# Kernel optimization log

Measured on AMD Instinct MI355X. Metric: run time of the kernel, lower is better.

Reference implementation:

```python
import jax, jax.numpy as jnp
import numpy as np

B, ENC, NCLUST = 8192, 256, 32


def setup_inputs() -> dict:
    key = jax.random.key(0)
    k1, k2 = jax.random.split(key)
    encodings = jax.random.normal(k1, (B, ENC), dtype=jnp.float32)
    logits = jax.random.normal(k2, (B, NCLUST), dtype=jnp.float32) * 2.0
    categorical = jax.nn.softmax(logits, axis=1)
    return {"encodings": encodings, "categorical": categorical, "k": 25}


def reference(encodings, categorical, k):
    """Vectorized ClusterOverlap training-path math.

    Original layer is an identity on encodings; the regularizer/metric is the
    per-sample neighbourhood entropy weighted by cluster confidence. We return
    that [B] vector (the compute of interest; reduce_mean of it is the loss).
    """
    hard_groups = jnp.argmax(categorical, axis=1)          # [B] int
    max_groups = jnp.max(categorical, axis=1)              # [B]

    # Pairwise Euclidean distances via the GEMM identity (fused cdist).
    sq = jnp.sum(encodings * encodings, axis=1)            # [B]
    d2 = sq[:, None] + sq[None, :] - 2.0 * (encodings @ encodings.T)
    dist = jnp.sqrt(jnp.maximum(d2, 0.0))                  # [B, B]

    # max_distance = sort(distances)[k]; neighbourhood = distances < max_distance
    thr = jnp.sort(dist, axis=1)[:, k]                     # [B]
    mask = (dist < thr[:, None]).astype(jnp.float32)       # [B, B]
    n_neigh = jnp.sum(mask, axis=1)                        # [B] (~k, incl. self)

    # bincount of neighbour cluster ids per row: mask @ one_hot(hard_groups)
    onehot = jax.nn.one_hot(hard_groups, categorical.shape[1], dtype=jnp.float32)
    counts = mask @ onehot                                 # [B, C]
    bins = counts / n_neigh[:, None]
    entropy = -jnp.sum(bins * jnp.log(bins + 1e-5), axis=1)  # [B]

    return entropy * max_groups
```

## Files before the change

kernel.cpp:

```cpp
#include <hip/hip_runtime.h>
#include <math.h>

#define BN 8192
#define ENC 256
#define NCL 32
#define BM 256
#define BK 32
#define CCAP 1024
#define SCOL 2048
#define SN 256
#define RCAP 24

typedef __attribute__((ext_vector_type(8))) short short8;
typedef __attribute__((ext_vector_type(4))) float f32x4;
typedef __attribute__((ext_vector_type(4))) unsigned uint4v;

__device__ __forceinline__ ushort f2bf(float x) {
    unsigned b = __float_as_uint(x);
    return (ushort)((b + 0x7FFFu + ((b >> 16) & 1u)) >> 16);
}

__device__ __forceinline__ void async16(void* lds, const void* g) {
    __builtin_amdgcn_global_load_lds(
        (const __attribute__((address_space(1))) unsigned*)g,
        (__attribute__((address_space(3))) unsigned*)lds, 16, 0, 0);
}

__global__ void prep_kernel(const float* __restrict__ enc, const float* __restrict__ cat,
                            float* __restrict__ sq, float* __restrict__ maxg,
                            int* __restrict__ hard, ushort* __restrict__ eh,
                            ushort* __restrict__ el, int* __restrict__ ccnt) {
    int w = threadIdx.x >> 6, l = threadIdx.x & 63;
    int row = blockIdx.x * 4 + w;
    int gid = blockIdx.x * 256 + threadIdx.x;
    if (gid < BN) ccnt[gid] = 0;

    const float4* e4 = (const float4*)(enc + (size_t)row * ENC);
    float4 v = e4[l];
    float s = v.x * v.x + v.y * v.y + v.z * v.z + v.w * v.w;
    for (int m = 32; m; m >>= 1) s += __shfl_xor(s, m, 64);

    ushort4 hh, ll;
    hh.x = f2bf(v.x); ll.x = f2bf(v.x - __uint_as_float((unsigned)hh.x << 16));
    hh.y = f2bf(v.y); ll.y = f2bf(v.y - __uint_as_float((unsigned)hh.y << 16));
    hh.z = f2bf(v.z); ll.z = f2bf(v.z - __uint_as_float((unsigned)hh.z << 16));
    hh.w = f2bf(v.w); ll.w = f2bf(v.w - __uint_as_float((unsigned)hh.w << 16));
    int g = l >> 1;
    int gs = (g & ~3) | ((g & 3) ^ ((row >> 1) & 3));
    int kp = gs * 8 + (l & 1) * 4;
    *(ushort4*)(eh + (size_t)row * ENC + kp) = hh;
    *(ushort4*)(el + (size_t)row * ENC + kp) = ll;

    float cv = (l < NCL) ? cat[(size_t)row * NCL + l] : -__builtin_huge_valf();
    int ci = (l < NCL) ? l : 0x7fffffff;
    for (int m = 32; m; m >>= 1) {
        float ov = __shfl_xor(cv, m, 64);
        int oi = __shfl_xor(ci, m, 64);
        if (ov > cv || (ov == cv && oi < ci)) { cv = ov; ci = oi; }
    }
    if (l == 0) { sq[row] = s; maxg[row] = cv; hard[row] = ci; }
}

__global__ __launch_bounds__(512, 2)
void dist_mfma_kernel(const ushort* __restrict__ eh, const ushort* __restrict__ el,
                      const float* __restrict__ sq, int mode,
                      float* __restrict__ samp, const unsigned* __restrict__ piv,
                      unsigned* __restrict__ cval, int* __restrict__ cidxb,
                      int* __restrict__ ccnt) {
    __shared__ __align__(16) ushort lds0[2][4 * BM * BK];

    int t = threadIdx.x, l = t & 63;
    int w = t >> 6;
    int wm = w >> 2, wn = w & 3;

    int bx, by;
    if (mode) {
        int gx = gridDim.x;
        int bid = blockIdx.y * gx + blockIdx.x;
        int xcd = bid & 7, i = bid >> 3;
        int strip = gx >> 3;
        bx = xcd * strip + (i % strip);
        by = i / strip;
    } else { bx = blockIdx.x; by = blockIdx.y; }

    int gi0 = by * BM;
    int j0 = (mode ? 0 : SCOL) + bx * BM;

    f32x4 acc[8][4];
#pragma unroll
    for (int m = 0; m < 8; ++m)
#pragma unroll
        for (int n = 0; n < 4; ++n) acc[m][n] = (f32x4){0.f, 0.f, 0.f, 0.f};

    int srow = t >> 2;
    int sg = (t & 3) * 8;
    int il = l & 15;

#define STAGE(BUF, K0)                                                        \
    do {                                                                      \
        _Pragma("unroll") for (int q_ = 0; q_ < 2; ++q_) {                    \
            int r_ = srow + q_ * 128;                                         \
            size_t ga_ = (size_t)(gi0 + r_) * ENC + (K0) + sg;                \
            size_t gb_ = (size_t)(j0 + r_) * ENC + (K0) + sg;                 \
            int ldo_ = r_ * BK + sg;                                          \
            async16(&lds0[BUF][0 * BM * BK + ldo_], eh + ga_);                \
            async16(&lds0[BUF][1 * BM * BK + ldo_], el + ga_);                \
            async16(&lds0[BUF][2 * BM * BK + ldo_], eh + gb_);                \
            async16(&lds0[BUF][3 * BM * BK + ldo_], el + gb_);                \
        }                                                                     \
    } while (0)

    STAGE(0, 0);
    __syncthreads();

#pragma unroll
    for (int ks = 0; ks < 8; ++ks) {
        int cb = ks & 1;
        if (ks + 1 < 8) STAGE(cb ^ 1, (ks + 1) * BK);

        const ushort* Ah = &lds0[cb][0];
        const ushort* Al = Ah + BM * BK;
        const ushort* Bh = Ah + 2 * BM * BK;
        const ushort* Bl = Ah + 3 * BM * BK;

        short8 bh[4], bl4[4];
#pragma unroll
        for (int n = 0; n < 4; ++n) {
            int R = wn * 64 + n * 16 + il;
            int gl = (l >> 4) ^ ((R >> 1) & 3);
            bh[n]  = *(const short8*)(Bh + R * BK + gl * 8);
            bl4[n] = *(const short8*)(Bl + R * BK + gl * 8);
        }
#pragma unroll
        for (int m = 0; m < 8; ++m) {
            int Ra = wm * 128 + m * 16 + il;
            int gla = (l >> 4) ^ ((Ra >> 1) & 3);
            short8 am  = *(const short8*)(Ah + Ra * BK + gla * 8);
            short8 alm = *(const short8*)(Al + Ra * BK + gla * 8);
#pragma unroll
            for (int n = 0; n < 4; ++n) {
                acc[m][n] = __builtin_amdgcn_mfma_f32_16x16x32_bf16(bh[n],  am,  acc[m][n], 0, 0, 0);
                acc[m][n] = __builtin_amdgcn_mfma_f32_16x16x32_bf16(bl4[n], am,  acc[m][n], 0, 0, 0);
                acc[m][n] = __builtin_amdgcn_mfma_f32_16x16x32_bf16(bh[n],  alm, acc[m][n], 0, 0, 0);
            }
        }

        __syncthreads();
    }
#undef STAGE

    int q4 = (l >> 4) * 4;
    float sqi[8];
    float sqj[4][4];
#pragma unroll
    for (int m = 0; m < 8; ++m) sqi[m] = sq[gi0 + wm * 128 + m * 16 + il];
#pragma unroll
    for (int n = 0; n < 4; ++n)
#pragma unroll
        for (int r = 0; r < 4; ++r) sqj[n][r] = sq[j0 + wn * 64 + n * 16 + q4 + r];

    if (!mode) {
#pragma unroll
        for (int m = 0; m < 8; ++m)
#pragma unroll
            for (int n = 0; n < 4; ++n) {
                float4 o;
                o.x = fmaxf(sqi[m] + sqj[n][0] - 2.f * acc[m][n][0], 0.f);
                o.y = fmaxf(sqi[m] + sqj[n][1] - 2.f * acc[m][n][1], 0.f);
                o.z = fmaxf(sqi[m] + sqj[n][2] - 2.f * acc[m][n][2], 0.f);
                o.w = fmaxf(sqi[m] + sqj[n][3] - 2.f * acc[m][n][3], 0.f);
                int row = gi0 + wm * 128 + m * 16 + il;
                int jc = j0 + wn * 64 + n * 16 + q4;
                *(float4*)(samp + (size_t)row * SN + (jc - SCOL)) = o;
            }
        return;
    }

    int* rcnt = (int*)&lds0[0][0];
    int* rbase = rcnt + BM;
    unsigned* bval = (unsigned*)(rbase + BM);
    int* bidx = (int*)(bval + BM * RCAP);

    if (t < BM) rcnt[t] = 0;
    unsigned pv[8];
#pragma unroll
    for (int m = 0; m < 8; ++m) pv[m] = piv[gi0 + wm * 128 + m * 16 + il];
    __syncthreads();

#pragma unroll
    for (int m = 0; m < 8; ++m)
#pragma unroll
        for (int n = 0; n < 4; ++n) {
            int lr = wm * 128 + m * 16 + il;
            int jc = j0 + wn * 64 + n * 16 + q4;
#pragma unroll
            for (int r = 0; r < 4; ++r) {
                float o = fmaxf(sqi[m] + sqj[n][r] - 2.f * acc[m][n][r], 0.f);
                unsigned ub = __float_as_uint(o);
                if (ub < pv[m]) {
                    int pos = atomicAdd(&rcnt[lr], 1);
                    if (pos < RCAP) {
                        bval[lr * RCAP + pos] = ub;
                        bidx[lr * RCAP + pos] = jc + r;
                    } else {
                        int slot = atomicAdd(&ccnt[gi0 + lr], 1);
                        if (slot < CCAP) {
                            cval[(size_t)(gi0 + lr) * CCAP + slot] = ub;
                            cidxb[(size_t)(gi0 + lr) * CCAP + slot] = jc + r;
                        }
                    }
                }
            }
        }
    __syncthreads();

    if (t < BM) {
        int c = rcnt[t]; if (c > RCAP) c = RCAP;
        rbase[t] = c ? atomicAdd(&ccnt[gi0 + t], c) : 0;
    }
    __syncthreads();

    {
        int lr = t >> 1;
        int c = rcnt[lr]; if (c > RCAP) c = RCAP;
        int b = rbase[lr];
        for (int e = t & 1; e < c; e += 2) {
            int s = b + e;
            if (s < CCAP) {
                cval[(size_t)(gi0 + lr) * CCAP + s] = bval[lr * RCAP + e];
                cidxb[(size_t)(gi0 + lr) * CCAP + s] = bidx[lr * RCAP + e];
            }
        }
    }
}

__global__ void pivot_kernel(const float* __restrict__ samp, const int* __restrict__ kptr,
                             unsigned* __restrict__ piv) {
    int w = threadIdx.x >> 6, l = threadIdx.x & 63;
    int row = blockIdx.x * 4 + w;
    const uint4v* rd = (const uint4v*)(samp + (size_t)row * SN);
    uint4v sv = rd[l];

    int topn = *kptr + 1;
    int r = topn / 16 + 1; if (r < 8) r = 8;

    unsigned lo = 0u, hi = 0x7F800000u;
    while (lo < hi) {
        unsigned mid = lo + ((hi - lo) >> 1);
        int c = 0;
#pragma unroll
        for (int e = 0; e < 4; ++e) c += __popcll(__ballot(sv[e] <= mid));
        if (c >= r) hi = mid; else lo = mid + 1;
    }
    if (l == 0) piv[row] = lo;
}

__global__ __launch_bounds__(256, 2)
void select_kernel(const unsigned* __restrict__ cval, const int* __restrict__ cidxb,
                   const int* __restrict__ ccnt, const unsigned* __restrict__ piv,
                   const float* __restrict__ enc, const float* __restrict__ sq,
                   const float* __restrict__ maxg, const int* __restrict__ hard,
                   const int* __restrict__ kptr, float* __restrict__ out) {
    __shared__ __align__(16) unsigned sval[CCAP];
    __shared__ int sidx[CCAP];
    __shared__ __align__(16) unsigned rowbuf[BN];
    __shared__ __align__(16) float encrow[ENC];
    __shared__ int scnt[2][4];
    __shared__ int sbins[NCL];

    int t = threadIdx.x, w = t >> 6, l = t & 63;
    int li = blockIdx.x;
    if (t < NCL) sbins[t] = 0;

    int topn = *kptr + 1;
    int nc = ccnt[li];
    bool ok = (nc >= topn) && (nc <= CCAP);
    unsigned thr;

    if (ok) {
#pragma unroll
        for (int k2 = 0; k2 < 4; ++k2) sval[t + k2 * 256] = 0xFFFFFFFFu;
        for (int pos = t; pos < nc; pos += 256) {
            sval[pos] = cval[(size_t)li * CCAP + pos];
            sidx[pos] = cidxb[(size_t)li * CCAP + pos];
        }
        __syncthreads();

        int pp = 0;
        unsigned lo = 0u, hi = piv[li];
        while (lo < hi) {
            unsigned mid = lo + ((hi - lo) >> 1);
            uint4v cv = ((const uint4v*)sval)[t];
            int cnt = 0;
#pragma unroll
            for (int c = 0; c < 4; ++c) cnt += __popcll(__ballot(cv[c] <= mid));
            if (l == 0) scnt[pp][w] = cnt;
            __syncthreads();
            int tot = scnt[pp][0] + scnt[pp][1] + scnt[pp][2] + scnt[pp][3];
            if (tot >= topn) hi = mid; else lo = mid + 1;
            pp ^= 1;
        }
        thr = lo;

        for (int pos = t; pos < nc; pos += 256)
            if (sval[pos] < thr) atomicAdd(&sbins[hard[sidx[pos]]], 1);
    } else {
        if (t < 64) ((float4*)encrow)[t] = ((const float4*)(enc + (size_t)li * ENC))[t];
        __syncthreads();
        float sqi = sq[li];
        for (int c0 = 0; c0 < BN; c0 += 256) {
            int c = c0 + t;
            const float* ec = enc + (size_t)c * ENC;
            float dot = 0.f;
            for (int d = 0; d < ENC; ++d) dot = fmaf(encrow[d], ec[d], dot);
            rowbuf[c] = __float_as_uint(fmaxf(sqi + sq[c] - 2.f * dot, 0.f));
        }
        __syncthreads();

        int pp = 0;
        unsigned lo = 0u, hi = 0x7F800000u;
        while (lo < hi) {
            unsigned mid = lo + ((hi - lo) >> 1);
            int cnt = 0;
#pragma unroll
            for (int q = 0; q < 8; ++q) {
                uint4v u = ((const uint4v*)rowbuf)[q * 256 + t];
#pragma unroll
                for (int c = 0; c < 4; ++c) cnt += __popcll(__ballot(u[c] <= mid));
            }
            if (l == 0) scnt[pp][w] = cnt;
            __syncthreads();
            int tot = scnt[pp][0] + scnt[pp][1] + scnt[pp][2] + scnt[pp][3];
            if (tot >= topn) hi = mid; else lo = mid + 1;
            pp ^= 1;
        }
        thr = lo;

#pragma unroll
        for (int q = 0; q < 8; ++q) {
            uint4v u = ((const uint4v*)rowbuf)[q * 256 + t];
#pragma unroll
            for (int c = 0; c < 4; ++c)
                if (u[c] < thr)
                    atomicAdd(&sbins[hard[(q * 256 + t) * 4 + c]], 1);
        }
    }
    __syncthreads();

    if (t < NCL) {
        int cnt = sbins[t];
        int n = cnt;
        for (int m = 16; m; m >>= 1) n += __shfl_xor(n, m, 64);
        float nf = (float)n;
        float b = (float)cnt / nf;
        float term = -b * logf(b + 1e-5f);
        for (int m = 16; m; m >>= 1) term += __shfl_xor(term, m, 64);
        if (t == 0) out[li] = term * maxg[li];
    }
}

extern "C" void kernel_launch(void* const* d_in, const int* in_sizes, int n_in,
                              void* d_out, int out_size, void* d_ws, size_t ws_size,
                              hipStream_t stream) {
    const float* enc = (const float*)d_in[0];
    const float* cat = (const float*)d_in[1];
    const int* kptr = (const int*)d_in[2];
    float* out = (float*)d_out;

    float* sq = (float*)d_ws;
    float* maxg = sq + BN;
    int* hard = (int*)(maxg + BN);
    ushort* eh = (ushort*)(hard + BN);
    ushort* el = eh + (size_t)BN * ENC;
    float* samp = (float*)(el + (size_t)BN * ENC);
    unsigned* piv = (unsigned*)(samp + (size_t)BN * SN);
    int* ccnt = (int*)(piv + BN);
    unsigned* cval = (unsigned*)(ccnt + BN);
    int* cidxb = (int*)(cval + (size_t)BN * CCAP);

    prep_kernel<<<BN / 4, 256, 0, stream>>>(enc, cat, sq, maxg, hard, eh, el, ccnt);

    dim3 gs(SN / BM, BN / BM);
    dist_mfma_kernel<<<gs, 512, 0, stream>>>(eh, el, sq, 0, samp, piv, cval, cidxb, ccnt);

    pivot_kernel<<<BN / 4, 256, 0, stream>>>(samp, kptr, piv);

    dim3 gm(BN / BM, BN / BM);
    dist_mfma_kernel<<<gm, 512, 0, stream>>>(eh, el, sq, 1, samp, piv, cval, cidxb, ccnt);

    select_kernel<<<BN, 256, 0, stream>>>(cval, cidxb, ccnt, piv, enc, sq,
                                          maxg, hard, kptr, out);
}
```

Measured before the change: 315.4 us.

## Interleave GEMM LDS reads with async staging; one wave per row in select

The main distance GEMM loop is split into four phases. Each phase reads a pair of A fragments from LDS, issues half of the next tile's async global-to-LDS loads, and then runs an MFMA cluster at raised wave priority, with explicit barriers and waitcnts placed between phases. This spreads load issue across the compute instead of issuing it all up front. The select kernel now handles four rows per block, one wave per row, keeping candidates in registers and counting with wave-local ballots in place of block-wide barriers. Rows whose candidate count is out of range fall back to a serial per-block full-row path, which adds risk if there are many such rows.

```diff
diff --git a/kernel.cpp b/kernel.cpp
--- a/kernel.cpp
+++ b/kernel.cpp
@@ -96,28 +96,64 @@
     int sg = (t & 3) * 8;
     int il = l & 15;
 
-#define STAGE(BUF, K0)                                                        \
+#define STAGE_A(BUF, K0)                                                      \
     do {                                                                      \
         _Pragma("unroll") for (int q_ = 0; q_ < 2; ++q_) {                    \
             int r_ = srow + q_ * 128;                                         \
             size_t ga_ = (size_t)(gi0 + r_) * ENC + (K0) + sg;                \
-            size_t gb_ = (size_t)(j0 + r_) * ENC + (K0) + sg;                 \
             int ldo_ = r_ * BK + sg;                                          \
             async16(&lds0[BUF][0 * BM * BK + ldo_], eh + ga_);                \
             async16(&lds0[BUF][1 * BM * BK + ldo_], el + ga_);                \
+        }                                                                     \
+    } while (0)
+#define STAGE_B(BUF, K0)                                                      \
+    do {                                                                      \
+        _Pragma("unroll") for (int q_ = 0; q_ < 2; ++q_) {                    \
+            int r_ = srow + q_ * 128;                                         \
+            size_t gb_ = (size_t)(j0 + r_) * ENC + (K0) + sg;                 \
+            int ldo_ = r_ * BK + sg;                                          \
             async16(&lds0[BUF][2 * BM * BK + ldo_], eh + gb_);                \
             async16(&lds0[BUF][3 * BM * BK + ldo_], el + gb_);                \
         }                                                                     \
     } while (0)
 
-    STAGE(0, 0);
+#define READ_APAIR(PH, AHp, ALp)                                              \
+    short8 a##PH##h0, a##PH##h1, a##PH##l0, a##PH##l1;                        \
+    do {                                                                      \
+        int Ra0 = wm * 128 + (2 * PH) * 16 + il;                              \
+        int Ra1 = Ra0 + 16;                                                   \
+        int g0 = (l >> 4) ^ ((Ra0 >> 1) & 3);                                 \
+        int g1 = (l >> 4) ^ ((Ra1 >> 1) & 3);                                 \
+        a##PH##h0 = *(const short8*)(AHp + Ra0 * BK + g0 * 8);                \
+        a##PH##h1 = *(const short8*)(AHp + Ra1 * BK + g1 * 8);                \
+        a##PH##l0 = *(const short8*)(ALp + Ra0 * BK + g0 * 8);                \
+        a##PH##l1 = *(const short8*)(ALp + Ra1 * BK + g1 * 8);                \
+    } while (0)
+
+#define CLUSTER(PH)                                                           \
+    do {                                                                      \
+        _Pragma("unroll") for (int n_ = 0; n_ < 4; ++n_) {                    \
+            acc[2*PH][n_]   = __builtin_amdgcn_mfma_f32_16x16x32_bf16(bh[n_],  a##PH##h0, acc[2*PH][n_],   0, 0, 0); \
+            acc[2*PH][n_]   = __builtin_amdgcn_mfma_f32_16x16x32_bf16(bl4[n_], a##PH##h0, acc[2*PH][n_],   0, 0, 0); \
+            acc[2*PH][n_]   = __builtin_amdgcn_mfma_f32_16x16x32_bf16(bh[n_],  a##PH##l0, acc[2*PH][n_],   0, 0, 0); \
+            acc[2*PH+1][n_] = __builtin_amdgcn_mfma_f32_16x16x32_bf16(bh[n_],  a##PH##h1, acc[2*PH+1][n_], 0, 0, 0); \
+            acc[2*PH+1][n_] = __builtin_amdgcn_mfma_f32_16x16x32_bf16(bl4[n_], a##PH##h1, acc[2*PH+1][n_], 0, 0, 0); \
+            acc[2*PH+1][n_] = __builtin_amdgcn_mfma_f32_16x16x32_bf16(bh[n_],  a##PH##l1, acc[2*PH+1][n_], 0, 0, 0); \
+        }                                                                     \
+    } while (0)
+
+#define BAR()     __builtin_amdgcn_s_barrier()
+#define LGKM0()   do { asm volatile("s_waitcnt lgkmcnt(0)" ::: "memory");     \
+                       __builtin_amdgcn_sched_barrier(0); } while (0)
+#define VM0()     asm volatile("s_waitcnt vmcnt(0)" ::: "memory")
+
+    STAGE_A(0, 0);
+    STAGE_B(0, 0);
     __syncthreads();
 
 #pragma unroll
     for (int ks = 0; ks < 8; ++ks) {
-        int cb = ks & 1;
-        if (ks + 1 < 8) STAGE(cb ^ 1, (ks + 1) * BK);
-
+        const int cb = ks & 1, nb = cb ^ 1;
         const ushort* Ah = &lds0[cb][0];
         const ushort* Al = Ah + BM * BK;
         const ushort* Bh = Ah + 2 * BM * BK;
@@ -131,23 +167,30 @@
             bh[n]  = *(const short8*)(Bh + R * BK + gl * 8);
             bl4[n] = *(const short8*)(Bl + R * BK + gl * 8);
         }
-#pragma unroll
-        for (int m = 0; m < 8; ++m) {
-            int Ra = wm * 128 + m * 16 + il;
-            int gla = (l >> 4) ^ ((Ra >> 1) & 3);
-            short8 am  = *(const short8*)(Ah + Ra * BK + gla * 8);
-            short8 alm = *(const short8*)(Al + Ra * BK + gla * 8);
-#pragma unroll
-            for (int n = 0; n < 4; ++n) {
-                acc[m][n] = __builtin_amdgcn_mfma_f32_16x16x32_bf16(bh[n],  am,  acc[m][n], 0, 0, 0);
-                acc[m][n] = __builtin_amdgcn_mfma_f32_16x16x32_bf16(bl4[n], am,  acc[m][n], 0, 0, 0);
-                acc[m][n] = __builtin_amdgcn_mfma_f32_16x16x32_bf16(bh[n],  alm, acc[m][n], 0, 0, 0);
-            }
-        }
-
-        __syncthreads();
-    }
-#undef STAGE
+        READ_APAIR(0, Ah, Al);
+        if (ks + 1 < 8) STAGE_A(nb, (ks + 1) * BK);
+        BAR(); LGKM0();
+        __builtin_amdgcn_s_setprio(1); CLUSTER(0); __builtin_amdgcn_s_setprio(0);
+        BAR();
+        READ_APAIR(1, Ah, Al);
+        if (ks + 1 < 8) STAGE_B(nb, (ks + 1) * BK);
+        BAR(); LGKM0();
+        __builtin_amdgcn_s_setprio(1); CLUSTER(1); __builtin_amdgcn_s_setprio(0);
+        BAR();
+        READ_APAIR(2, Ah, Al);
+        BAR(); LGKM0();
+        __builtin_amdgcn_s_setprio(1); CLUSTER(2); __builtin_amdgcn_s_setprio(0);
+        BAR();
+        READ_APAIR(3, Ah, Al);
+        BAR(); LGKM0();
+        __builtin_amdgcn_s_setprio(1); CLUSTER(3); __builtin_amdgcn_s_setprio(0);
+        if (ks + 1 < 8) VM0();
+        BAR();
+    }
+#undef STAGE_A
+#undef STAGE_B
+#undef READ_APAIR
+#undef CLUSTER
 
     int q4 = (l >> 4) * 4;
     float sqi[8];
@@ -261,53 +304,53 @@
                    const float* __restrict__ enc, const float* __restrict__ sq,
                    const float* __restrict__ maxg, const int* __restrict__ hard,
                    const int* __restrict__ kptr, float* __restrict__ out) {
-    __shared__ __align__(16) unsigned sval[CCAP];
-    __shared__ int sidx[CCAP];
     __shared__ __align__(16) unsigned rowbuf[BN];
     __shared__ __align__(16) float encrow[ENC];
     __shared__ int scnt[2][4];
-    __shared__ int sbins[NCL];
+    __shared__ int sbins[4][NCL];
+    __shared__ int sfail;
 
     int t = threadIdx.x, w = t >> 6, l = t & 63;
-    int li = blockIdx.x;
-    if (t < NCL) sbins[t] = 0;
+    int li = blockIdx.x * 4 + w;
+    if (t == 0) sfail = 0;
+    if (l < NCL) sbins[w][l] = 0;
+    __syncthreads();
 
     int topn = *kptr + 1;
     int nc = ccnt[li];
     bool ok = (nc >= topn) && (nc <= CCAP);
-    unsigned thr;
 
     if (ok) {
-#pragma unroll
-        for (int k2 = 0; k2 < 4; ++k2) sval[t + k2 * 256] = 0xFFFFFFFFu;
-        for (int pos = t; pos < nc; pos += 256) {
-            sval[pos] = cval[(size_t)li * CCAP + pos];
-            sidx[pos] = cidxb[(size_t)li * CCAP + pos];
-        }
-        __syncthreads();
-
-        int pp = 0;
+        unsigned cv[16]; int cidx[16];
+#pragma unroll
+        for (int j = 0; j < 16; ++j) {
+            int idx = j * 64 + l;
+            bool v = idx < nc;
+            cv[j]   = v ? cval[(size_t)li * CCAP + idx] : 0xFFFFFFFFu;
+            cidx[j] = v ? cidxb[(size_t)li * CCAP + idx] : 0;
+        }
         unsigned lo = 0u, hi = piv[li];
         while (lo < hi) {
             unsigned mid = lo + ((hi - lo) >> 1);
-            uint4v cv = ((const uint4v*)sval)[t];
             int cnt = 0;
 #pragma unroll
-            for (int c = 0; c < 4; ++c) cnt += __popcll(__ballot(cv[c] <= mid));
-            if (l == 0) scnt[pp][w] = cnt;
-            __syncthreads();
-            int tot = scnt[pp][0] + scnt[pp][1] + scnt[pp][2] + scnt[pp][3];
-            if (tot >= topn) hi = mid; else lo = mid + 1;
-            pp ^= 1;
-        }
-        thr = lo;
-
-        for (int pos = t; pos < nc; pos += 256)
-            if (sval[pos] < thr) atomicAdd(&sbins[hard[sidx[pos]]], 1);
+            for (int j = 0; j < 16; ++j) cnt += __popcll(__ballot(cv[j] <= mid));
+            if (cnt >= topn) hi = mid; else lo = mid + 1;
+        }
+#pragma unroll
+        for (int j = 0; j < 16; ++j)
+            if (cv[j] < lo) atomicAdd(&sbins[w][hard[cidx[j]]], 1);
     } else {
-        if (t < 64) ((float4*)encrow)[t] = ((const float4*)(enc + (size_t)li * ENC))[t];
+        if (l == 0) atomicOr(&sfail, 1 << w);
+    }
+    __syncthreads();
+    int fmask = sfail;
+
+    for (int fw = 0; fw < 4; ++fw) if (fmask & (1 << fw)) {
+        int li2 = blockIdx.x * 4 + fw;
+        if (t < 64) ((float4*)encrow)[t] = ((const float4*)(enc + (size_t)li2 * ENC))[t];
         __syncthreads();
-        float sqi = sq[li];
+        float sqi = sq[li2];
         for (int c0 = 0; c0 < BN; c0 += 256) {
             int c = c0 + t;
             const float* ec = enc + (size_t)c * ENC;
@@ -316,7 +359,6 @@
             rowbuf[c] = __float_as_uint(fmaxf(sqi + sq[c] - 2.f * dot, 0.f));
         }
         __syncthreads();
-
         int pp = 0;
         unsigned lo = 0u, hi = 0x7F800000u;
         while (lo < hi) {
@@ -334,28 +376,26 @@
             if (tot >= topn) hi = mid; else lo = mid + 1;
             pp ^= 1;
         }
-        thr = lo;
-
 #pragma unroll
         for (int q = 0; q < 8; ++q) {
             uint4v u = ((const uint4v*)rowbuf)[q * 256 + t];
 #pragma unroll
             for (int c = 0; c < 4; ++c)
-                if (u[c] < thr)
-                    atomicAdd(&sbins[hard[(q * 256 + t) * 4 + c]], 1);
-        }
-    }
-    __syncthreads();
-
-    if (t < NCL) {
-        int cnt = sbins[t];
+                if (u[c] < lo)
+                    atomicAdd(&sbins[fw][hard[(q * 256 + t) * 4 + c]], 1);
+        }
+        __syncthreads();
+    }
+
+    if (l < NCL) {
+        int cnt = sbins[w][l];
         int n = cnt;
         for (int m = 16; m; m >>= 1) n += __shfl_xor(n, m, 64);
         float nf = (float)n;
         float b = (float)cnt / nf;
         float term = -b * logf(b + 1e-5f);
         for (int m = 16; m; m >>= 1) term += __shfl_xor(term, m, 64);
-        if (t == 0) out[li] = term * maxg[li];
+        if (l == 0) out[li] = term * maxg[li];
     }
 }
 
@@ -388,6 +428,6 @@
     dim3 gm(BN / BM, BN / BM);
     dist_mfma_kernel<<<gm, 512, 0, stream>>>(eh, el, sq, 1, samp, piv, cval, cidxb, ccnt);
 
-    select_kernel<<<BN, 256, 0, stream>>>(cval, cidxb, ccnt, piv, enc, sq,
-                                          maxg, hard, kptr, out);
-}
+    select_kernel<<<BN / 4, 256, 0, stream>>>(cval, cidxb, ccnt, piv, enc, sq,
+                                              maxg, hard, kptr, out);
+}
```

New measurement: 258.4 us. 1.22x faster.
